# Kernel tuning notes

Hardware: AMD Instinct MI355X
Metric: run time of the kernel (lower is better)

Reference implementation:

```python
import jax, jax.numpy as jnp
import numpy as np

L, B, T, I, H, O = 2, 64, 256, 512, 1024, 256
HIDDEN_WEIGHT = 0.5  # placement_weight = 1 - hidden_weight
# dropout is identity in eval mode (reference is deterministic)


def setup_inputs() -> dict:
    key = jax.random.key(0)
    ks = jax.random.split(key, 20)
    def unif(k, shape, fan):
        b = 1.0 / np.sqrt(fan)
        return jax.random.uniform(k, shape, jnp.float32, -b, b)
    lengths = jax.random.randint(ks[4], (B,), 0, T + 1)
    lengths = lengths.at[0].set(T).at[1].set(0)  # exercise full-length and zero-length paths
    return {
        "step_input": jax.random.normal(ks[0], (B, T, I), jnp.float32),
        "clstm_hidden": jax.random.normal(ks[1], (B, H), jnp.float32),
        "hidden": jax.random.normal(ks[2], (L, B, H), jnp.float32),
        "cell": jax.random.normal(ks[3], (L, B, H), jnp.float32),
        "input_lengths": lengths.astype(jnp.int64),
        # LSTM params, PyTorch gate order [i, f, g, o]
        "w_ih0": unif(ks[5], (4 * H, I), H), "w_hh0": unif(ks[6], (4 * H, H), H),
        "b_ih0": unif(ks[7], (4 * H,), H), "b_hh0": unif(ks[8], (4 * H,), H),
        "w_ih1": unif(ks[9], (4 * H, H), H), "w_hh1": unif(ks[10], (4 * H, H), H),
        "b_ih1": unif(ks[11], (4 * H,), H), "b_hh1": unif(ks[12], (4 * H,), H),
        "w1": unif(ks[13], (H, H), H), "b1": unif(ks[14], (H,), H),
        "w2": unif(ks[15], (O, H), H), "b2": unif(ks[16], (O,), H),
    }


def compute_weighted_hidden(clstm_hidden, hidden, lens):
    # vectorized version of the per-(layer,batch) min-max rescale loop
    cmin = jnp.min(clstm_hidden, axis=-1, keepdims=True)            # [B,1]
    crange = jnp.max(clstm_hidden, axis=-1, keepdims=True) - cmin   # [B,1]
    safe_cr = jnp.where(crange > 0, crange, 1.0)
    s = jnp.where(crange > 0, (clstm_hidden - cmin) / safe_cr, clstm_hidden)  # [B,H]
    hmin = jnp.min(hidden, axis=-1, keepdims=True)                  # [L,B,1]
    hrange = jnp.max(hidden, axis=-1, keepdims=True) - hmin         # [L,B,1]
    s2 = jnp.where(hrange > 0, hmin + s[None] * hrange,
                   jnp.broadcast_to(s[None], hidden.shape))         # [L,B,H]
    c = jnp.where((lens == 0)[None, :, None], clstm_hidden[None], s2)
    return HIDDEN_WEIGHT * hidden + (1.0 - HIDDEN_WEIGHT) * c


def lstm_forward(x, h0, c0, lens, layer_params):
    # x: [B,T,I]; h0,c0: [L,B,H]; lens already clamped to >=1
    t_idx = jnp.arange(x.shape[1])

    def step(carry, xt_t):
        h, c = carry                      # each [L,B,H]
        xt, t = xt_t                      # xt: [B,I]
        valid = (t < lens)[:, None]       # [B,1]
        inp = xt
        hs, cs = [], []
        for l, (wih, whh, bih, bhh) in enumerate(layer_params):
            gates = inp @ wih.T + bih + h[l] @ whh.T + bhh   # [B,4H]
            i, f, g, o = jnp.split(gates, 4, axis=-1)
            i, f, o = jax.nn.sigmoid(i), jax.nn.sigmoid(f), jax.nn.sigmoid(o)
            g = jnp.tanh(g)
            c_new = f * c[l] + i * g
            h_new = o * jnp.tanh(c_new)
            hs.append(jnp.where(valid, h_new, h[l]))
            cs.append(jnp.where(valid, c_new, c[l]))
            inp = jnp.where(valid, h_new, 0.0)
        out_t = inp                        # top layer output, zeroed on padding
        return (jnp.stack(hs), jnp.stack(cs)), out_t

    (hn, cn), outs = jax.lax.scan(step, (h0, c0), (x.transpose(1, 0, 2), t_idx))
    return outs.transpose(1, 0, 2), hn, cn  # [B,T,H], [L,B,H], [L,B,H]


def reference(step_input, clstm_hidden, hidden, cell, input_lengths,
              w_ih0, w_hh0, b_ih0, b_hh0, w_ih1, w_hh1, b_ih1, b_hh1,
              w1, b1, w2, b2):
    weighted_hidden = compute_weighted_hidden(clstm_hidden, hidden, input_lengths)
    lens = jnp.clip(input_lengths, 1, None)  # torch.clamp(min=1)
    layer_params = [(w_ih0, w_hh0, b_ih0, b_hh0), (w_ih1, w_hh1, b_ih1, b_hh1)]
    lstm_out, hn, cn = lstm_forward(step_input, weighted_hidden, cell, lens, layer_params)
    # dropout layers are identity in eval mode
    h1 = jax.nn.relu(lstm_out @ w1.T + b1)
    logits = jax.nn.relu(h1 @ w2.T + b2)  # [B,T,O]
    zero = (input_lengths == 0)
    logits = jnp.where(zero[:, None, None], 0.0, logits)
    hn = jnp.where(zero[None, :, None], 0.0, hn)
    cn = jnp.where(zero[None, :, None], 0.0, cn)
    return logits, hn, cn
```

## Files before the change

### kernel.cpp

```cpp
#include <hip/hip_runtime.h>


typedef __bf16 bf16x8 __attribute__((ext_vector_type(8)));
typedef float f32x4 __attribute__((ext_vector_type(4)));
typedef int i32x4 __attribute__((ext_vector_type(4)));

__device__ __forceinline__ unsigned short f2bf(float f) {
  unsigned u = __float_as_uint(f);
  u = u + 0x7FFFu + ((u >> 16) & 1u);
  return (unsigned short)(u >> 16);
}
__device__ __forceinline__ float sigm_(float x) { return 1.f / (1.f + __expf(-x)); }
__device__ __forceinline__ float tanh_(float x) { return 1.f - 2.f / (__expf(2.f * x) + 1.f); }

__device__ __forceinline__ int hxoff(int b, int u) {
  return (b >> 4) * 16384 + (u >> 5) * 512 + ((u >> 3) & 3) * 128 + (b & 15) * 8 + (u & 7);
}

__global__ void cvt_kernel(const float* __restrict__ s, unsigned short* __restrict__ d, int n) {
  int i = (blockIdx.x * 256 + threadIdx.x) * 4;
  if (i < n) {
    float4 v = *reinterpret_cast<const float4*>(s + i);
    ushort4 o = make_ushort4(f2bf(v.x), f2bf(v.y), f2bf(v.z), f2bf(v.w));
    *reinterpret_cast<ushort4*>(d + i) = o;
  }
}

__global__ __launch_bounds__(256) void prep_kernel(
    const float* __restrict__ clstm, const float* __restrict__ hidden,
    const float* __restrict__ cell, const int* __restrict__ lens,
    float* __restrict__ hstate, float* __restrict__ cstate,
    unsigned short* __restrict__ h0buf, unsigned short* __restrict__ h1buf,
    const float* __restrict__ bih0, const float* __restrict__ bhh0,
    const float* __restrict__ bih1, const float* __restrict__ bhh1,
    float* __restrict__ bias0, float* __restrict__ bias1p,
    unsigned* __restrict__ bar) {
  const int tid = threadIdx.x, blk = blockIdx.x;
  const int l = blk >> 6, b = blk & 63;
  const float* crow = clstm + b * 1024;
  const float* hrow = hidden + ((size_t)l * 64 + b) * 1024;
  float cmn = 3.4e38f, cmx = -3.4e38f, hmn = 3.4e38f, hmx = -3.4e38f;
  for (int i = tid; i < 1024; i += 256) {
    float c = crow[i], h = hrow[i];
    cmn = fminf(cmn, c); cmx = fmaxf(cmx, c);
    hmn = fminf(hmn, h); hmx = fmaxf(hmx, h);
  }
#pragma unroll
  for (int off = 32; off > 0; off >>= 1) {
    cmn = fminf(cmn, __shfl_xor(cmn, off));
    cmx = fmaxf(cmx, __shfl_xor(cmx, off));
    hmn = fminf(hmn, __shfl_xor(hmn, off));
    hmx = fmaxf(hmx, __shfl_xor(hmx, off));
  }
  __shared__ float red[4][4];
  int wv = tid >> 6;
  if ((tid & 63) == 0) { red[wv][0] = cmn; red[wv][1] = cmx; red[wv][2] = hmn; red[wv][3] = hmx; }
  __syncthreads();
  cmn = fminf(fminf(red[0][0], red[1][0]), fminf(red[2][0], red[3][0]));
  cmx = fmaxf(fmaxf(red[0][1], red[1][1]), fmaxf(red[2][1], red[3][1]));
  hmn = fminf(fminf(red[0][2], red[1][2]), fminf(red[2][2], red[3][2]));
  hmx = fmaxf(fmaxf(red[0][3], red[1][3]), fmaxf(red[2][3], red[3][3]));
  const float crange = cmx - cmn, hrange = hmx - hmn;
  const int len = lens[b];
  const size_t base = ((size_t)l * 64 + b) * 1024;
  unsigned short* dst = (l == 0) ? h0buf : (h1buf + 65536);
  for (int i = tid; i < 1024; i += 256) {
    float cv = crow[i], hv = hrow[i];
    float s = (crange > 0.f) ? (cv - cmn) / crange : cv;
    float s2 = (hrange > 0.f) ? (hmn + s * hrange) : s;
    float cc = (len == 0) ? cv : s2;
    float w = 0.5f * hv + 0.5f * cc;
    hstate[base + i] = w;
    cstate[base + i] = cell[base + i];
    dst[hxoff(b, i)] = f2bf(w);
  }
  if (blk == 0) {
    for (int n = tid; n < 4096; n += 256) {
      bias0[n] = bih0[n] + bhh0[n];
      bias1p[(n & 1023) * 4 + (n >> 10)] = bih1[n] + bhh1[n];
      bar[n] = 0u;
    }
  }
}

template <int AMODE, int EPI>
__global__ __launch_bounds__(256) void gemm_kernel(
    const void* __restrict__ Ap, const unsigned short* __restrict__ Bw,
    void* __restrict__ Cout, const float* __restrict__ bias,
    const int* __restrict__ lens, int M, int N, int K, int t0) {
  __shared__ unsigned short Al[128][40];
  __shared__ unsigned short Bl[128][40];
  const int tid = threadIdx.x;
  const int m0 = blockIdx.y * 128, n0 = blockIdx.x * 128;
  const int srow = tid >> 2;
  const int c8 = (tid & 3) * 8;
  size_t aoff0, aoff1;
  {
    int r = m0 + srow, r2 = r + 64;
    if (AMODE == 0) {
      aoff0 = (size_t)r * K; aoff1 = (size_t)r2 * K;
    } else {
      aoff0 = ((size_t)(r & 63) * 256 + t0 + (r >> 6)) * K;
      aoff1 = ((size_t)(r2 & 63) * 256 + t0 + (r2 >> 6)) * K;
    }
  }
  const size_t boff0 = (size_t)(n0 + srow) * K, boff1 = (size_t)(n0 + srow + 64) * K;
  const int wave = tid >> 6, lane = tid & 63, ln = lane & 15, quad = lane >> 4;
  const int mq = (wave >> 1) * 64, nq = (wave & 1) * 64;
  f32x4 acc[4][4] = {};
  const int nkt = K >> 5;
  for (int kt = 0; kt < nkt; ++kt) {
    const int kc = kt * 32 + c8;
    if (AMODE == 1) {
      const float* A = (const float*)Ap;
      const float* p0 = A + aoff0 + kc;
      const float* p1 = A + aoff1 + kc;
      float4 v0 = *reinterpret_cast<const float4*>(p0);
      float4 v0b = *reinterpret_cast<const float4*>(p0 + 4);
      float4 v1 = *reinterpret_cast<const float4*>(p1);
      float4 v1b = *reinterpret_cast<const float4*>(p1 + 4);
      *reinterpret_cast<ushort4*>(&Al[srow][c8]) =
          make_ushort4(f2bf(v0.x), f2bf(v0.y), f2bf(v0.z), f2bf(v0.w));
      *reinterpret_cast<ushort4*>(&Al[srow][c8 + 4]) =
          make_ushort4(f2bf(v0b.x), f2bf(v0b.y), f2bf(v0b.z), f2bf(v0b.w));
      *reinterpret_cast<ushort4*>(&Al[srow + 64][c8]) =
          make_ushort4(f2bf(v1.x), f2bf(v1.y), f2bf(v1.z), f2bf(v1.w));
      *reinterpret_cast<ushort4*>(&Al[srow + 64][c8 + 4]) =
          make_ushort4(f2bf(v1b.x), f2bf(v1b.y), f2bf(v1b.z), f2bf(v1b.w));
    } else {
      const unsigned short* A = (const unsigned short*)Ap;
      *reinterpret_cast<int4*>(&Al[srow][c8]) = *reinterpret_cast<const int4*>(A + aoff0 + kc);
      *reinterpret_cast<int4*>(&Al[srow + 64][c8]) = *reinterpret_cast<const int4*>(A + aoff1 + kc);
    }
    *reinterpret_cast<int4*>(&Bl[srow][c8]) = *reinterpret_cast<const int4*>(Bw + boff0 + kc);
    *reinterpret_cast<int4*>(&Bl[srow + 64][c8]) = *reinterpret_cast<const int4*>(Bw + boff1 + kc);
    __syncthreads();
    bf16x8 af[4], bfr[4];
#pragma unroll
    for (int i = 0; i < 4; ++i) {
      af[i] = *reinterpret_cast<const bf16x8*>(&Al[mq + i * 16 + ln][quad * 8]);
      bfr[i] = *reinterpret_cast<const bf16x8*>(&Bl[nq + i * 16 + ln][quad * 8]);
    }
#pragma unroll
    for (int i = 0; i < 4; ++i)
#pragma unroll
      for (int j = 0; j < 4; ++j)
        acc[i][j] = __builtin_amdgcn_mfma_f32_16x16x32_bf16(af[i], bfr[j], acc[i][j], 0, 0, 0);
    __syncthreads();
  }
#pragma unroll
  for (int i = 0; i < 4; ++i) {
    int mmb = m0 + mq + i * 16 + quad * 4;
#pragma unroll
    for (int j = 0; j < 4; ++j) {
      int nn = n0 + nq + j * 16 + ln;
      float bv = bias[nn];
#pragma unroll
      for (int r = 0; r < 4; ++r) {
        int mm = mmb + r;
        float v = acc[i][j][r] + bv;
        if (EPI >= 1) v = fmaxf(v, 0.f);
        if (EPI == 2) {
          if (lens[mm >> 8] == 0) v = 0.f;
          ((float*)Cout)[(size_t)mm * N + nn] = v;
        } else if (EPI == 1) {
          ((unsigned short*)Cout)[(size_t)mm * N + nn] = f2bf(v);
        } else {
          size_t idx = ((size_t)mm * 128 + ((nn >> 3) & 127)) * 32 + (nn & 7) * 4 + (nn >> 10);
          ((float*)Cout)[idx] = v;
        }
      }
    }
  }
}

#define HLo(dst, ptr, off) \
  asm volatile("global_load_dwordx4 %0, %1, off offset:" off " sc0 sc1" \
               : "=v"(dst) : "v"(ptr))
#define HL4(h0, h1, h2, h3, ptr) \
  HLo(h0, ptr, "0"); HLo(h1, ptr, "1024"); HLo(h2, ptr, "2048"); HLo(h3, ptr, "3072")
#define HLF(dst, ptr) \
  asm volatile("global_load_dwordx4 %0, %1, off sc0 sc1" : "=v"(dst) : "v"(ptr))
#define HST(ptr, val) \
  asm volatile("global_store_dwordx4 %0, %1, off sc0 sc1" :: "v"(ptr), "v"(val) : "memory")

__global__ __launch_bounds__(512) void rec2_kernel(
    const unsigned short* __restrict__ whh0b,
    const unsigned short* __restrict__ wih1b,
    const unsigned short* __restrict__ whh1b,
    const float* __restrict__ G2,
    const float* __restrict__ bias1p,
    unsigned short* __restrict__ h0buf,
    unsigned short* __restrict__ h1buf,
    float* __restrict__ pre1buf,
    float* __restrict__ hstate, float* __restrict__ cstate,
    unsigned short* __restrict__ h1out,
    const int* __restrict__ lens, int t0, int nint, unsigned* __restrict__ bar) {
  __shared__ unsigned short wlds[32 * 1032];
  __shared__ float glds[2][64][73];
  __shared__ unsigned short hsh[64][16];
  const int tid = threadIdx.x;
  const int bid = blockIdx.x;
  const bool isL1 = bid >= 128;
  const int g = bid & 127;
  {
    int r = tid >> 4;
    int c0 = (tid & 15) * 64;
    const unsigned short* src;
    if (!isL1)
      src = wih1b + (size_t)((r >> 3) * 1024 + g * 8 + (r & 7)) * 1024;
    else
      src = whh1b + (size_t)((2 + (r >> 4)) * 1024 + g * 16 + (r & 15)) * 1024;
    const i32x4* s4 = reinterpret_cast<const i32x4*>(src + c0);
    i32x4* dst = reinterpret_cast<i32x4*>(wlds + r * 1032 + c0);
#pragma unroll
    for (int j = 0; j < 8; ++j) dst[j] = s4[j];
  }
  const int wave = tid >> 6, lane = tid & 63, ln = lane & 15, quad = lane >> 4;
  const int mt = wave & 3, kw = wave >> 2;
  bf16x8 bregA[16], bregB[16];
  {
    const unsigned short *bpA, *bpB;
    if (!isL1) {
      bpA = whh0b + (size_t)((ln >> 3) * 1024 + g * 8 + (ln & 7)) * 1024 + kw * 512 + quad * 8;
      bpB = whh0b + (size_t)((2 + (ln >> 3)) * 1024 + g * 8 + (ln & 7)) * 1024 + kw * 512 + quad * 8;
    } else {
      bpA = whh1b + (size_t)(g * 16 + ln) * 1024 + kw * 512 + quad * 8;
      bpB = whh1b + (size_t)(1024 + g * 16 + ln) * 1024 + kw * 512 + quad * 8;
    }
#pragma unroll
    for (int kt = 0; kt < 16; ++kt) {
      bregA[kt] = *reinterpret_cast<const bf16x8*>(bpA + kt * 32);
      bregB[kt] = *reinterpret_cast<const bf16x8*>(bpB + kt * 32);
    }
  }
  const int b = tid >> 3, ul = tid & 7;
  const size_t sb0 = (size_t)(isL1 ? 65536 : 0) + (size_t)b * 1024 +
                     (isL1 ? g * 16 + ul : g * 8 + ul);
  float cm0 = cstate[sb0], hm0 = hstate[sb0];
  float cm1 = 0.f, hm1 = 0.f;
  if (isL1) { cm1 = cstate[sb0 + 8]; hm1 = hstate[sb0 + 8]; }
  int lv0 = lens[b];
  const int len = lv0 < 1 ? 1 : lv0;
  int lvA = lens[mt * 16 + ln];
  const int lenmA = lvA < 1 ? 1 : lvA;
  f32x4 b1a = {0.f, 0.f, 0.f, 0.f}, b1b = {0.f, 0.f, 0.f, 0.f};
  if (isL1) {
    b1a = *reinterpret_cast<const f32x4*>(bias1p + (g * 16 + ul) * 4);
    b1b = *reinterpret_cast<const f32x4*>(bias1p + (g * 16 + 8 + ul) * 4);
  }
  int lenp = 257;
  if (isL1 && tid < 128) { int lv = lens[tid >> 1]; lenp = lv < 1 ? 1 : lv; }
  const int puboff = (tid >> 4) * 16384 + (g >> 2) * 512 + (g & 3) * 128 + (tid & 15) * 8;
  const int pub1off = ((tid >> 1) >> 4) * 16384 + (g >> 1) * 512 +
                      ((g * 2 + (tid & 1)) & 3) * 128 + ((tid >> 1) & 15) * 8;
  const bf16x8 z8 = {};
  const i32x4 zi = {};
  __syncthreads();

  for (int k = 0; k < nint; ++k) {
    const int s = t0 + k;
    const bool actG = (!isL1) && (k < 64);
    const bool actP = (!isL1) && (s >= 1) && (s <= 256);
    const bool actL = isL1 && (s >= 2);
    if (actG || actP || actL) {
      f32x4 pga = {0.f, 0.f, 0.f, 0.f}, pgb = {0.f, 0.f, 0.f, 0.f};
      if (isL1) {
        const float* pr = pre1buf + (size_t)(s & 1) * 262144 +
                          ((size_t)b * 1024 + g * 16) * 4;
        HLF(pga, pr + ul * 4);
        HLF(pgb, pr + (8 + ul) * 4);
      }
      bf16x8 hf[16];
      const unsigned short* p = (isL1 ? h1buf + ((s - 1) & 1) * 65536
                                      : h0buf + (s & 1) * 65536) +
                                mt * 16384 + kw * 8192 + lane * 8;
      HL4(hf[0], hf[1], hf[2], hf[3], p);
      HL4(hf[4], hf[5], hf[6], hf[7], p + 2048);
      HL4(hf[8], hf[9], hf[10], hf[11], p + 4096);
      HL4(hf[12], hf[13], hf[14], hf[15], p + 6144);
      if (actG)
        pga = *reinterpret_cast<const f32x4*>(
            G2 + (((size_t)(k * 64 + b)) * 128 + g) * 32 + ul * 4);
      const bool maskA = (!isL1) && ((s - 1) >= lenmA);
      f32x4 acc0 = {0.f, 0.f, 0.f, 0.f}, acc1 = acc0, acc2 = acc0, acc3 = acc0;
      const unsigned short* wp = wlds + ln * 1032 + kw * 512 + quad * 8;
      asm volatile("s_waitcnt vmcnt(8)" ::: "memory");
      __builtin_amdgcn_sched_barrier(0);
#pragma unroll
      for (int kt = 0; kt < 8; ++kt) {
        const unsigned short* c = wp + kt * 32;
        bf16x8 bC = *reinterpret_cast<const bf16x8*>(c);
        bf16x8 bD = *reinterpret_cast<const bf16x8*>(c + 16512);
        bf16x8 a_ = hf[kt];
        acc0 = __builtin_amdgcn_mfma_f32_16x16x32_bf16(a_, bregA[kt], acc0, 0, 0, 0);
        acc1 = __builtin_amdgcn_mfma_f32_16x16x32_bf16(a_, bregB[kt], acc1, 0, 0, 0);
        bf16x8 am = maskA ? z8 : a_;
        acc2 = __builtin_amdgcn_mfma_f32_16x16x32_bf16(am, bC, acc2, 0, 0, 0);
        acc3 = __builtin_amdgcn_mfma_f32_16x16x32_bf16(am, bD, acc3, 0, 0, 0);
      }
      asm volatile("s_waitcnt vmcnt(0)" ::: "memory");
      __builtin_amdgcn_sched_barrier(0);
#pragma unroll
      for (int kt = 8; kt < 16; ++kt) {
        const unsigned short* c = wp + kt * 32;
        bf16x8 bC = *reinterpret_cast<const bf16x8*>(c);
        bf16x8 bD = *reinterpret_cast<const bf16x8*>(c + 16512);
        bf16x8 a_ = hf[kt];
        acc0 = __builtin_amdgcn_mfma_f32_16x16x32_bf16(a_, bregA[kt], acc0, 0, 0, 0);
        acc1 = __builtin_amdgcn_mfma_f32_16x16x32_bf16(a_, bregB[kt], acc1, 0, 0, 0);
        bf16x8 am = maskA ? z8 : a_;
        acc2 = __builtin_amdgcn_mfma_f32_16x16x32_bf16(am, bC, acc2, 0, 0, 0);
        acc3 = __builtin_amdgcn_mfma_f32_16x16x32_bf16(am, bD, acc3, 0, 0, 0);
      }
#pragma unroll
      for (int r = 0; r < 4; ++r) {
        float* gp = &glds[kw][mt * 16 + quad * 4 + r][0];
        gp[ln] = acc0[r]; gp[16 + ln] = acc1[r];
        gp[32 + ln] = acc2[r]; gp[48 + ln] = acc3[r];
      }
      __syncthreads();
      const float* g0 = &glds[0][b][0];
      const float* g1 = &glds[1][b][0];
      if (actG) {
        float pi = g0[ul] + g1[ul] + pga.x;
        float pf = g0[8 + ul] + g1[8 + ul] + pga.y;
        float pgg = g0[16 + ul] + g1[16 + ul] + pga.z;
        float po = g0[24 + ul] + g1[24 + ul] + pga.w;
        float ig = sigm_(pi), fg = sigm_(pf), gv = tanh_(pgg), og = sigm_(po);
        float cn_ = fg * cm0 + ig * gv;
        float hn_ = og * tanh_(cn_);
        if (s < len) { cm0 = cn_; hm0 = hn_; }
        hsh[b][ul] = f2bf(hm0);
      }
      if (actP) {
        f32x4 pv;
        pv.x = g0[32 + ul] + g1[32 + ul];
        pv.y = g0[40 + ul] + g1[40 + ul];
        pv.z = g0[48 + ul] + g1[48 + ul];
        pv.w = g0[56 + ul] + g1[56 + ul];
        float* pd = pre1buf + (size_t)((s - 1) & 1) * 262144 +
                    (size_t)b * 4096 + g * 32 + ul * 4;
        HST(pd, pv);
      }
      if (actL) {
        {
          float pi = g0[ul] + g1[ul] + pga.x + b1a.x;
          float pf = g0[16 + ul] + g1[16 + ul] + pga.y + b1a.y;
          float pgg = g0[32 + ul] + g1[32 + ul] + pga.z + b1a.z;
          float po = g0[48 + ul] + g1[48 + ul] + pga.w + b1a.w;
          float ig = sigm_(pi), fg = sigm_(pf), gv = tanh_(pgg), og = sigm_(po);
          float cn_ = fg * cm0 + ig * gv;
          float hn_ = og * tanh_(cn_);
          if (s - 2 < len) { cm0 = cn_; hm0 = hn_; }
          hsh[b][ul] = f2bf(hm0);
        }
        {
          int iu = 8 + ul;
          float pi = g0[iu] + g1[iu] + pgb.x + b1b.x;
          float pf = g0[16 + iu] + g1[16 + iu] + pgb.y + b1b.y;
          float pgg = g0[32 + iu] + g1[32 + iu] + pgb.z + b1b.z;
          float po = g0[48 + iu] + g1[48 + iu] + pgb.w + b1b.w;
          float ig = sigm_(pi), fg = sigm_(pf), gv = tanh_(pgg), og = sigm_(po);
          float cn_ = fg * cm1 + ig * gv;
          float hn_ = og * tanh_(cn_);
          if (s - 2 < len) { cm1 = cn_; hm1 = hn_; }
          hsh[b][iu] = f2bf(hm1);
        }
      }
      __syncthreads();
      if (!isL1) {
        if (actG && tid < 64) {
          i32x4 v = *reinterpret_cast<const i32x4*>(&hsh[tid][0]);
          unsigned short* d = h0buf + ((s + 1) & 1) * 65536 + puboff;
          HST(d, v);
        }
        asm volatile("s_waitcnt vmcnt(0)" ::: "memory");
      } else {
        if (tid < 128) {
          const int pb = tid >> 1, half = tid & 1;
          i32x4 v = *reinterpret_cast<const i32x4*>(&hsh[pb][half * 8]);
          unsigned short* d = h1buf + (s & 1) * 65536 + pub1off;
          HST(d, v);
          const int t = s - 2;
          i32x4 vo = (t < lenp) ? v : zi;
          *reinterpret_cast<i32x4*>(h1out + ((size_t)pb * 256 + t) * 1024 +
                                    g * 16 + half * 8) = vo;
          asm volatile("s_waitcnt vmcnt(1)" ::: "memory");
        }
      }
    }
    __syncthreads();
    if (tid == 0) {
      unsigned a = __hip_atomic_fetch_add(bar + ((bid >> 3) << 4), 1u,
                                          __ATOMIC_RELAXED, __HIP_MEMORY_SCOPE_AGENT);
      if ((a & 7u) == 7u) {
        const unsigned val = (unsigned)(s + 1);
        const int gi = bid >> 3;
#pragma unroll
        for (int rep = 0; rep < 8; ++rep)
          __hip_atomic_store(bar + 1024 + ((gi * 8 + rep) << 4), val,
                             __ATOMIC_RELAXED, __HIP_MEMORY_SCOPE_AGENT);
      }
    }
    if (tid < 24) {
      const unsigned tgt = (unsigned)(s + 1);
      while (__hip_atomic_load(bar + 1024 + ((tid * 8 + (bid & 7)) << 4),
                               __ATOMIC_RELAXED, __HIP_MEMORY_SCOPE_AGENT) < tgt)
        __builtin_amdgcn_s_sleep(2);
    }
    __syncthreads();
  }
  hstate[sb0] = hm0; cstate[sb0] = cm0;
  if (isL1) { hstate[sb0 + 8] = hm1; cstate[sb0 + 8] = cm1; }
}

__global__ void final_kernel(const float* __restrict__ hstate, const float* __restrict__ cstate,
                             const int* __restrict__ lens, float* __restrict__ out) {
  int i = blockIdx.x * 256 + threadIdx.x;
  int b = (i >> 10) & 63;
  float z = (lens[b] == 0) ? 0.f : 1.f;
  out[4194304 + i] = z * hstate[i];
  out[4325376 + i] = z * cstate[i];
}

extern "C" void kernel_launch(void* const* d_in, const int* in_sizes, int n_in,
                              void* d_out, int out_size, void* d_ws, size_t ws_size,
                              hipStream_t stream) {
  const float* x = (const float*)d_in[0];
  const float* clstm = (const float*)d_in[1];
  const float* hidden = (const float*)d_in[2];
  const float* cell = (const float*)d_in[3];
  const int* lens = (const int*)d_in[4];
  const float* wih0 = (const float*)d_in[5];
  const float* whh0 = (const float*)d_in[6];
  const float* bih0 = (const float*)d_in[7];
  const float* bhh0 = (const float*)d_in[8];
  const float* wih1 = (const float*)d_in[9];
  const float* whh1 = (const float*)d_in[10];
  const float* bih1 = (const float*)d_in[11];
  const float* bhh1 = (const float*)d_in[12];
  const float* w1 = (const float*)d_in[13];
  const float* b1 = (const float*)d_in[14];
  const float* w2 = (const float*)d_in[15];
  const float* b2 = (const float*)d_in[16];
  float* out = (float*)d_out;

  char* ws = (char*)d_ws;
  size_t off = 0;
  auto alloc = [&](size_t bytes) -> void* {
    void* p = ws + off;
    off += (bytes + 255) & ~(size_t)255;
    return p;
  };
  unsigned short* wih0_b = (unsigned short*)alloc(2097152ull * 2);
  unsigned short* whh0_b = (unsigned short*)alloc(4194304ull * 2);
  unsigned short* wih1_b = (unsigned short*)alloc(4194304ull * 2);
  unsigned short* whh1_b = (unsigned short*)alloc(4194304ull * 2);
  unsigned short* w1_b = (unsigned short*)alloc(1048576ull * 2);
  unsigned short* w2_b = (unsigned short*)alloc(262144ull * 2);
  float* bias0 = (float*)alloc(4096 * 4);
  float* bias1p = (float*)alloc(4096 * 4);
  float* hstate = (float*)alloc(131072ull * 4);
  float* cstate = (float*)alloc(131072ull * 4);
  unsigned short* h0buf = (unsigned short*)alloc(131072ull * 2);
  unsigned short* h1buf = (unsigned short*)alloc(131072ull * 2);
  float* pre1buf = (float*)alloc(524288ull * 4);
  unsigned* bar = (unsigned*)alloc(16384);
  float* G = (float*)alloc(16777216ull * 4);
  unsigned short* h1out = (unsigned short*)alloc(16777216ull * 2);

  cvt_kernel<<<2048, 256, 0, stream>>>(wih0, wih0_b, 2097152);
  cvt_kernel<<<4096, 256, 0, stream>>>(whh0, whh0_b, 4194304);
  cvt_kernel<<<4096, 256, 0, stream>>>(wih1, wih1_b, 4194304);
  cvt_kernel<<<4096, 256, 0, stream>>>(whh1, whh1_b, 4194304);
  cvt_kernel<<<1024, 256, 0, stream>>>(w1, w1_b, 1048576);
  cvt_kernel<<<256, 256, 0, stream>>>(w2, w2_b, 262144);

  prep_kernel<<<128, 256, 0, stream>>>(clstm, hidden, cell, lens, hstate, cstate,
                                       h0buf, h1buf, bih0, bhh0, bih1, bhh1,
                                       bias0, bias1p, bar);

  for (int c = 0; c < 4; ++c) {
    gemm_kernel<1, 0><<<dim3(32, 32), 256, 0, stream>>>(x, wih0_b, G, bias0, lens,
                                                        4096, 4096, 512, c * 64);
    rec2_kernel<<<192, 512, 0, stream>>>(whh0_b, wih1_b, whh1_b, G, bias1p,
                                         h0buf, h1buf, pre1buf, hstate, cstate,
                                         h1out, lens, c * 64, (c == 3) ? 66 : 64, bar);
  }
  gemm_kernel<0, 1><<<dim3(8, 128), 256, 0, stream>>>(h1out, w1_b, (void*)G, b1, lens,
                                                      16384, 1024, 1024, 0);
  gemm_kernel<0, 2><<<dim3(2, 128), 256, 0, stream>>>((const void*)G, w2_b, out, b2, lens,
                                                      16384, 256, 1024, 0);
  final_kernel<<<512, 256, 0, stream>>>(hstate, cstate, lens, out);
}
```

Baseline: 2.038 ms.

## Overlap next chunk's input GEMM with recurrence via extra blocks in rec2 kernel

Adds 64 extra blocks to the persistent recurrence kernel that compute the layer-0 input projection for the next 64-timestep chunk into a double-buffered G array. This hides the separate per-chunk GEMM launches behind the latency-bound recurrence. The risk is that the extra blocks compete with the recurrence blocks for CUs, bandwidth and LDS, and this could slow the grid-barrier-synchronised recurrence. It also doubles the G workspace.

```diff
diff --git a/kernel.cpp b/kernel.cpp
--- a/kernel.cpp
+++ b/kernel.cpp
@@ -195,12 +195,96 @@
     float* __restrict__ pre1buf,
     float* __restrict__ hstate, float* __restrict__ cstate,
     unsigned short* __restrict__ h1out,
-    const int* __restrict__ lens, int t0, int nint, unsigned* __restrict__ bar) {
+    const int* __restrict__ lens, int t0, int nint, unsigned* __restrict__ bar,
+    const float* __restrict__ xin,
+    const unsigned short* __restrict__ wih0bk,
+    float* __restrict__ Gnext,
+    const float* __restrict__ bias0k,
+    int t0n, int do_gemm) {
   __shared__ unsigned short wlds[32 * 1032];
   __shared__ float glds[2][64][73];
   __shared__ unsigned short hsh[64][16];
+  __shared__ unsigned short Ag[2][128][40];
+  __shared__ unsigned short Bg[2][128][40];
   const int tid = threadIdx.x;
   const int bid = blockIdx.x;
+
+  if (bid >= 192) {
+    if (!do_gemm) return;
+    const int w = bid - 192;
+    const int half = tid >> 8;
+    const int tl = tid & 255;
+    const int srow = tl >> 2;
+    const int c8 = (tl & 3) * 8;
+    const int wv = tl >> 6, lane2 = tl & 63, ln2 = lane2 & 15, qd = lane2 >> 4;
+    const int mq = (wv >> 1) * 64, nq = (wv & 1) * 64;
+    for (int it = 0; it < 8; ++it) {
+      const int tau = it * 128 + w * 2 + half;
+      const int m0 = (tau >> 5) * 128, n0 = (tau & 31) * 128;
+      size_t aoff0, aoff1;
+      {
+        int r = m0 + srow, r2 = r + 64;
+        aoff0 = ((size_t)(r & 63) * 256 + t0n + (r >> 6)) * 512;
+        aoff1 = ((size_t)(r2 & 63) * 256 + t0n + (r2 >> 6)) * 512;
+      }
+      const size_t boff0 = (size_t)(n0 + srow) * 512;
+      const size_t boff1 = (size_t)(n0 + srow + 64) * 512;
+      f32x4 acc[4][4] = {};
+#pragma unroll 1
+      for (int kt = 0; kt < 16; ++kt) {
+        const int kc = kt * 32 + c8;
+        const float* p0 = xin + aoff0 + kc;
+        const float* p1 = xin + aoff1 + kc;
+        float4 v0 = *reinterpret_cast<const float4*>(p0);
+        float4 v0b = *reinterpret_cast<const float4*>(p0 + 4);
+        float4 v1 = *reinterpret_cast<const float4*>(p1);
+        float4 v1b = *reinterpret_cast<const float4*>(p1 + 4);
+        *reinterpret_cast<ushort4*>(&Ag[half][srow][c8]) =
+            make_ushort4(f2bf(v0.x), f2bf(v0.y), f2bf(v0.z), f2bf(v0.w));
+        *reinterpret_cast<ushort4*>(&Ag[half][srow][c8 + 4]) =
+            make_ushort4(f2bf(v0b.x), f2bf(v0b.y), f2bf(v0b.z), f2bf(v0b.w));
+        *reinterpret_cast<ushort4*>(&Ag[half][srow + 64][c8]) =
+            make_ushort4(f2bf(v1.x), f2bf(v1.y), f2bf(v1.z), f2bf(v1.w));
+        *reinterpret_cast<ushort4*>(&Ag[half][srow + 64][c8 + 4]) =
+            make_ushort4(f2bf(v1b.x), f2bf(v1b.y), f2bf(v1b.z), f2bf(v1b.w));
+        *reinterpret_cast<int4*>(&Bg[half][srow][c8]) =
+            *reinterpret_cast<const int4*>(wih0bk + boff0 + kc);
+        *reinterpret_cast<int4*>(&Bg[half][srow + 64][c8]) =
+            *reinterpret_cast<const int4*>(wih0bk + boff1 + kc);
+        __syncthreads();
+        bf16x8 af[4], bfr[4];
+#pragma unroll
+        for (int i = 0; i < 4; ++i) {
+          af[i] = *reinterpret_cast<const bf16x8*>(&Ag[half][mq + i * 16 + ln2][qd * 8]);
+          bfr[i] = *reinterpret_cast<const bf16x8*>(&Bg[half][nq + i * 16 + ln2][qd * 8]);
+        }
+#pragma unroll
+        for (int i = 0; i < 4; ++i)
+#pragma unroll
+          for (int j = 0; j < 4; ++j)
+            acc[i][j] = __builtin_amdgcn_mfma_f32_16x16x32_bf16(af[i], bfr[j], acc[i][j], 0, 0, 0);
+        __syncthreads();
+      }
+#pragma unroll
+      for (int i = 0; i < 4; ++i) {
+        int mmb = m0 + mq + i * 16 + qd * 4;
+#pragma unroll
+        for (int j = 0; j < 4; ++j) {
+          int nn = n0 + nq + j * 16 + ln2;
+          float bv = bias0k[nn];
+#pragma unroll
+          for (int r = 0; r < 4; ++r) {
+            int mm = mmb + r;
+            float v = acc[i][j][r] + bv;
+            size_t idx = ((size_t)mm * 128 + ((nn >> 3) & 127)) * 32 + (nn & 7) * 4 + (nn >> 10);
+            Gnext[idx] = v;
+          }
+        }
+      }
+    }
+    return;
+  }
+
   const bool isL1 = bid >= 128;
   const int g = bid & 127;
   {
@@ -467,7 +551,8 @@
   unsigned short* h1buf = (unsigned short*)alloc(131072ull * 2);
   float* pre1buf = (float*)alloc(524288ull * 4);
   unsigned* bar = (unsigned*)alloc(16384);
-  float* G = (float*)alloc(16777216ull * 4);
+  float* G2a = (float*)alloc(16777216ull * 4);
+  float* G2b = (float*)alloc(16777216ull * 4);
   unsigned short* h1out = (unsigned short*)alloc(16777216ull * 2);
 
   cvt_kernel<<<2048, 256, 0, stream>>>(wih0, wih0_b, 2097152);
@@ -481,16 +566,20 @@
                                        h0buf, h1buf, bih0, bhh0, bih1, bhh1,
                                        bias0, bias1p, bar);
 
+  gemm_kernel<1, 0><<<dim3(32, 32), 256, 0, stream>>>(x, wih0_b, G2a, bias0, lens,
+                                                      4096, 4096, 512, 0);
   for (int c = 0; c < 4; ++c) {
-    gemm_kernel<1, 0><<<dim3(32, 32), 256, 0, stream>>>(x, wih0_b, G, bias0, lens,
-                                                        4096, 4096, 512, c * 64);
-    rec2_kernel<<<192, 512, 0, stream>>>(whh0_b, wih1_b, whh1_b, G, bias1p,
+    float* Gc = (c & 1) ? G2b : G2a;
+    float* Gn = (c & 1) ? G2a : G2b;
+    rec2_kernel<<<256, 512, 0, stream>>>(whh0_b, wih1_b, whh1_b, Gc, bias1p,
                                          h0buf, h1buf, pre1buf, hstate, cstate,
-                                         h1out, lens, c * 64, (c == 3) ? 66 : 64, bar);
-  }
-  gemm_kernel<0, 1><<<dim3(8, 128), 256, 0, stream>>>(h1out, w1_b, (void*)G, b1, lens,
+                                         h1out, lens, c * 64, (c == 3) ? 66 : 64, bar,
+                                         x, wih0_b, Gn, bias0, (c + 1) * 64,
+                                         (c < 3) ? 1 : 0);
+  }
+  gemm_kernel<0, 1><<<dim3(8, 128), 256, 0, stream>>>(h1out, w1_b, (void*)G2a, b1, lens,
                                                       16384, 1024, 1024, 0);
-  gemm_kernel<0, 2><<<dim3(2, 128), 256, 0, stream>>>((const void*)G, w2_b, out, b2, lens,
+  gemm_kernel<0, 2><<<dim3(2, 128), 256, 0, stream>>>((const void*)G2a, w2_b, out, b2, lens,
                                                       16384, 256, 1024, 0);
   final_kernel<<<512, 256, 0, stream>>>(hstate, cstate, lens, out);
 }
```

After: 1.878 ms. -7.9%, faster.
